# Performance work log

Measured on AMD Instinct MI355X. Metric: run time of the kernel, lower is better.

## Reference

```python
import jax, jax.numpy as jnp
import numpy as np

EMB_SZ = 1024
NUM_HEADS = 16
HEAD_SIZE = EMB_SZ // NUM_HEADS  # 64; inputs must have last dim == HEAD_SIZE (module quirk)
B, S = 2, 2048


def setup_inputs() -> dict:
    key = jax.random.key(0)
    ks = jax.random.split(key, 8)
    return {
        "inputs_for_keys": jax.random.normal(ks[0], (B, S, HEAD_SIZE), jnp.float32),
        "inputs_for_values": jax.random.normal(ks[1], (B, S, HEAD_SIZE), jnp.float32),
        "inputs_for_queries": jax.random.normal(ks[2], (B, S, HEAD_SIZE), jnp.float32),
        # per-head projection weights, stacked over heads (glorot-ish scale)
        "Wk": jax.random.normal(ks[3], (NUM_HEADS, HEAD_SIZE, HEAD_SIZE), jnp.float32) * 0.125,
        "Wv": jax.random.normal(ks[4], (NUM_HEADS, HEAD_SIZE, HEAD_SIZE), jnp.float32) * 0.125,
        "Wq": jax.random.normal(ks[5], (NUM_HEADS, HEAD_SIZE, HEAD_SIZE), jnp.float32) * 0.125,
        "Wo": jax.random.normal(ks[6], (EMB_SZ, EMB_SZ), jnp.float32) * 0.03,
        "bo": jnp.zeros((EMB_SZ,), jnp.float32),
    }


def reference(inputs_for_keys, inputs_for_values, inputs_for_queries, Wk, Wv, Wq, Wo, bo):
    # Each head sees the SAME full inputs (module quirk), distinct weights per head.
    K = jnp.einsum('bsd,hde->bhse', inputs_for_keys, Wk)      # [B,H,Sk,hs]
    V = jnp.einsum('bsd,hde->bhse', inputs_for_values, Wv)    # [B,H,Sk,hs]
    Q = jnp.einsum('bsd,hde->bhse', inputs_for_queries, Wq)   # [B,H,Sq,hs]

    Sq, Sk = Q.shape[2], K.shape[2]
    scores = jnp.einsum('bhqe,bhke->bhqk', Q, K)              # [B,H,Sq,Sk]
    # causal additive mask: -inf strictly above the diagonal (as in np.triu(..., k=1))
    mask = jnp.triu(jnp.full((Sq, Sk), -jnp.inf, dtype=scores.dtype), k=1)
    scale = jnp.asarray(Sk, scores.dtype) ** 0.5
    # NOTE: original divides AFTER adding the mask; -inf/scale == -inf so math matches
    attn = jax.nn.softmax((scores + mask) / scale, axis=-1)   # [B,H,Sq,Sk]

    heads = jnp.einsum('bhqk,bhke->bhqe', attn, V)            # [B,H,Sq,hs]
    # concat heads along last dim (head order matches the Python-loop concat)
    concat = heads.transpose(0, 2, 1, 3).reshape(heads.shape[0], Sq, -1)  # [B,Sq,emb]
    return concat @ Wo + bo                                   # Dense(emb_sz), linear activation
```

## Files before the change

kernel.cpp:

```cpp
#include <hip/hip_runtime.h>
#include <hip/hip_bf16.h>
#include <cstdint>

typedef unsigned short u16;
typedef __bf16 bf16x8 __attribute__((ext_vector_type(8)));
typedef u16 u16x8 __attribute__((ext_vector_type(8)));
typedef unsigned u32x4 __attribute__((ext_vector_type(4)));
typedef float f32x4 __attribute__((ext_vector_type(4)));
typedef float f32x16 __attribute__((ext_vector_type(16)));

#define B_ 2
#define S_ 2048
#define H_ 16
#define HS_ 64
#define EMB_ 1024
#define QSCALE 0.022097086912079608f
#define LOG2E  1.4426950408889634f

static __device__ __forceinline__ u16 f2bf(float f) {
  unsigned int u = __float_as_uint(f);
  u += 0x7fffu + ((u >> 16) & 1u);
  return (u16)(u >> 16);
}

static __device__ __forceinline__ float ex2(float x) {
#if __has_builtin(__builtin_amdgcn_exp2f)
  return __builtin_amdgcn_exp2f(x);
#else
  float r; asm("v_exp_f32 %0, %1" : "=v"(r) : "v"(x)); return r;
#endif
}

static __device__ __forceinline__ float tsum16(const f32x16& s) {
  float a0 = s[0] + s[1],  a1 = s[2] + s[3];
  float a2 = s[4] + s[5],  a3 = s[6] + s[7];
  float a4 = s[8] + s[9],  a5 = s[10] + s[11];
  float a6 = s[12] + s[13], a7 = s[14] + s[15];
  a0 += a1; a2 += a3; a4 += a5; a6 += a7;
  a0 += a2; a4 += a6;
  return a0 + a4;
}

static __device__ __forceinline__ f32x4 mfma16(u16x8 a, u16x8 b, f32x4 c) {
  return __builtin_amdgcn_mfma_f32_16x16x32_bf16(
      __builtin_bit_cast(bf16x8, a), __builtin_bit_cast(bf16x8, b), c, 0, 0, 0);
}
static __device__ __forceinline__ f32x16 mfma32(u16x8 a, u16x8 b, f32x16 c) {
  return __builtin_amdgcn_mfma_f32_32x32x16_bf16(
      __builtin_bit_cast(bf16x8, a), __builtin_bit_cast(bf16x8, b), c, 0, 0, 0);
}

static __device__ __forceinline__ char* swzb(void* base, int row, int colbyte) {
  return (char*)base + ((row * 128 + colbyte) ^ ((row & 7) << 4));
}
static __device__ __forceinline__ u16x8* swzp(void* base, int row, int colbyte) {
  return (u16x8*)swzb(base, row, colbyte);
}

static __device__ __forceinline__ void pk_swap(float a0, float a1, float b0, float b1,
                                               unsigned& x, unsigned& y) {
  unsigned A, Bv;
  asm("v_cvt_pk_bf16_f32 %0, %1, %2" : "=v"(A) : "v"(a0), "v"(a1));
  asm("v_cvt_pk_bf16_f32 %0, %1, %2" : "=v"(Bv) : "v"(b0), "v"(b1));
  asm("v_permlane32_swap_b32 %0, %1" : "+v"(A), "+v"(Bv));
  x = A; y = Bv;
}

__global__ __launch_bounds__(256) void k_transpose_wo(const float* __restrict__ Wo,
                                                      u16* __restrict__ Wot) {
  __shared__ __align__(16) u16 T[64][72];
  const int kb = blockIdx.y * 64, nb = blockIdx.x * 64;
  const int r = threadIdx.x >> 2;
  const int c0 = (threadIdx.x & 3) << 4;
  const float* src = Wo + (size_t)(kb + r) * EMB_ + nb + c0;
#pragma unroll
  for (int i = 0; i < 16; i += 4) {
    float4 f = *(const float4*)(src + i);
    T[c0 + i + 0][r] = f2bf(f.x);
    T[c0 + i + 1][r] = f2bf(f.y);
    T[c0 + i + 2][r] = f2bf(f.z);
    T[c0 + i + 3][r] = f2bf(f.w);
  }
  __syncthreads();
  u16* dst = Wot + (size_t)(nb + r) * EMB_ + kb + c0;
  *(u16x8*)(dst)     = *(const u16x8*)&T[r][c0];
  *(u16x8*)(dst + 8) = *(const u16x8*)&T[r][c0 + 8];
}

__global__ __launch_bounds__(256) void k_proj(
    const float* __restrict__ xq, const float* __restrict__ xk, const float* __restrict__ xv,
    const float* __restrict__ Wq, const float* __restrict__ Wk, const float* __restrict__ Wv,
    u16* __restrict__ Qf, u16* __restrict__ Kf, u16* __restrict__ Vf) {
  __shared__ __align__(16) u16 Xb[64][64];
  __shared__ __align__(16) u16 Wb[64][64];
  __shared__ __align__(16) u16 Tt[64][64];
  const int sb = blockIdx.x;
  const int bh = blockIdx.y;
  const int tn = blockIdx.z;
  const int b = bh >> 4, h = bh & 15;
  const int t = threadIdx.x;
  const int r = t >> 2, c0 = (t & 3) << 4;
  const int lane = t & 63, wv = t >> 6;
  const int lq = lane & 15, lg = lane >> 4;
  const int l31 = lane & 31, hi = lane >> 5;
  const float* xs = (tn == 0) ? xq : (tn == 1) ? xk : xv;
  const float* wsp3 = (tn == 0) ? Wq : (tn == 1) ? Wk : Wv;

  const float* src = xs + ((size_t)(b * S_ + sb * 64 + r)) * HS_ + c0;
#pragma unroll
  for (int i = 0; i < 16; i += 8) {
    float4 fa = *(const float4*)(src + i);
    float4 fb = *(const float4*)(src + i + 4);
    u16x8 v = {f2bf(fa.x), f2bf(fa.y), f2bf(fa.z), f2bf(fa.w),
               f2bf(fb.x), f2bf(fb.y), f2bf(fb.z), f2bf(fb.w)};
    *swzp(Xb, r, (c0 + i) * 2) = v;
  }
  const float* wsp = wsp3 + ((size_t)(h * HS_ + r)) * HS_ + c0;
#pragma unroll
  for (int i = 0; i < 16; i += 4) {
    float4 f = *(const float4*)(wsp + i);
    *(u16*)swzb(Wb, c0 + i + 0, r * 2) = f2bf(f.x);
    *(u16*)swzb(Wb, c0 + i + 1, r * 2) = f2bf(f.y);
    *(u16*)swzb(Wb, c0 + i + 2, r * 2) = f2bf(f.z);
    *(u16*)swzb(Wb, c0 + i + 3, r * 2) = f2bf(f.w);
  }
  __syncthreads();
  if (tn < 2) {
    u16x8 a0 = *swzp(Xb, wv * 16 + lq, lg * 16);
    u16x8 a1 = *swzp(Xb, wv * 16 + lq, 64 + lg * 16);
    const float osc = (tn == 0) ? (QSCALE * LOG2E) : 1.0f;
#pragma unroll
    for (int et = 0; et < 4; ++et) {
      u16x8 b0 = *swzp(Wb, et * 16 + lq, lg * 16);
      u16x8 b1 = *swzp(Wb, et * 16 + lq, 64 + lg * 16);
      f32x4 acc = {0.f, 0.f, 0.f, 0.f};
      acc = mfma16(a0, b0, acc);
      acc = mfma16(a1, b1, acc);
#pragma unroll
      for (int rr = 0; rr < 4; ++rr)
        *(u16*)swzb(Tt, wv * 16 + lg * 4 + rr, (et * 16 + lq) * 2) = f2bf(acc[rr] * osc);
    }
  } else {
    u16x8 xb0 = *swzp(Xb, wv * 16 + lq, lg * 16);
    u16x8 xb1 = *swzp(Xb, wv * 16 + lq, 64 + lg * 16);
#pragma unroll
    for (int et = 0; et < 4; ++et) {
      u16x8 a0 = *swzp(Wb, et * 16 + lq, lg * 16);
      u16x8 a1 = *swzp(Wb, et * 16 + lq, 64 + lg * 16);
      f32x4 acc = {0.f, 0.f, 0.f, 0.f};
      acc = mfma16(a0, xb0, acc);
      acc = mfma16(a1, xb1, acc);
#pragma unroll
      for (int rr = 0; rr < 4; ++rr)
        *(u16*)swzb(Tt, et * 16 + lg * 4 + rr, (wv * 16 + lq) * 2) = f2bf(acc[rr]);
    }
  }
  __syncthreads();
  if (tn < 2) {
    u16* dst = (tn == 0) ? Qf : Kf;
#pragma unroll
    for (int tl = 0; tl < 2; ++tl) {
      u16x8 v = *swzp(Tt, tl * 32 + l31, wv * 32 + hi * 16);
      size_t off = (((size_t)(bh * 64 + sb * 2 + tl)) * 4 + wv) * 512 + lane * 8;
      *(u16x8*)(dst + off) = v;
    }
  } else {
#pragma unroll
    for (int eta = 0; eta < 2; ++eta) {
      u16x8 v = *swzp(Tt, eta * 32 + l31, wv * 32 + hi * 16);
      size_t off = ((((size_t)(bh * 32 + sb)) * 2 + eta) * 4 + wv) * 512 + lane * 8;
      *(u16x8*)(Vf + off) = v;
    }
  }
}

__global__ __launch_bounds__(128, 2) void k_attn(
    const u16* __restrict__ Qf, const u16* __restrict__ Kf, const u16* __restrict__ Vf,
    u16* __restrict__ Co) {
  __shared__ float Xch[64][33];
  __shared__ __align__(16) u16 Osw[32][64];
  const int bid = blockIdx.x;
  const int xcd = bid & 7, idx = bid >> 3;
  const int bh = (xcd << 2) | (idx & 3);
  const int pr = idx >> 2;
  const int b = bh >> 4, h = bh & 15;
  const int w = threadIdx.x >> 6;
  const int l = threadIdx.x & 63;
  const int lq = l & 31, hi = l >> 5;
  const float NEG = -3.0e38f;

  const u16* Kbase = Kf + ((size_t)(bh * 64) * 4) * 512 + l * 8;
  const u16* Vbase = Vf + ((size_t)(bh * 32) * 8) * 512 + l * 8;

#pragma unroll 1
  for (int ph = 0; ph < 2; ++ph) {
    const int t = ph ? (63 - pr) : pr;
    const int qg = t * 32 + lq;
    const int n = (t >> 1) + 1;
    const int mid = n >> 1;
    const int jbeg = w ? mid : 0;
    const int jhot = w ? (n - 1) : mid;

    const u16* Qbase = Qf + (((size_t)(bh * 64 + t)) * 4) * 512 + l * 8;
    u16x8 qf[4];
#pragma unroll
    for (int ss = 0; ss < 4; ++ss) qf[ss] = *(const u16x8*)(Qbase + ss * 512);

    f32x16 o0, o1;
#pragma unroll
    for (int r = 0; r < 16; ++r) { o0[r] = 0.f; o1[r] = 0.f; }
    float ll = 0.f;

    u16x8 kl[4], kh[4], vl[4], vh[4];
    {
      const u16* pk = Kbase + (size_t)jbeg * 8 * 512;
      const u16* pv = Vbase + (size_t)jbeg * 8 * 512;
#pragma unroll
      for (int ss = 0; ss < 4; ++ss) {
        kl[ss] = *(const u16x8*)(pk + ss * 512);
        kh[ss] = *(const u16x8*)(pk + (4 + ss) * 512);
        vl[ss] = *(const u16x8*)(pv + ss * 512);
        vh[ss] = *(const u16x8*)(pv + (4 + ss) * 512);
      }
    }

    for (int j = jbeg; j < jhot; ++j) {
      f32x16 s0, s1;
#pragma unroll
      for (int r = 0; r < 16; ++r) { s0[r] = -16.f; s1[r] = -16.f; }
      __builtin_amdgcn_s_setprio(1);
      s0 = mfma32(kl[0], qf[0], s0);
      s0 = mfma32(kl[1], qf[1], s0);
      s0 = mfma32(kl[2], qf[2], s0);
      s0 = mfma32(kl[3], qf[3], s0);
      s1 = mfma32(kh[0], qf[0], s1);
      s1 = mfma32(kh[1], qf[1], s1);
      s1 = mfma32(kh[2], qf[2], s1);
      s1 = mfma32(kh[3], qf[3], s1);
      __builtin_amdgcn_s_setprio(0);
      {
        const u16* pk = Kbase + (size_t)(j + 1) * 8 * 512;
#pragma unroll
        for (int ss = 0; ss < 4; ++ss) {
          kl[ss] = *(const u16x8*)(pk + ss * 512);
          kh[ss] = *(const u16x8*)(pk + (4 + ss) * 512);
        }
      }
#pragma unroll
      for (int r = 0; r < 16; ++r) s0[r] = ex2(s0[r]);
#pragma unroll
      for (int r = 0; r < 16; ++r) s1[r] = ex2(s1[r]);
      u16x8 pf0, pf1, pf2, pf3;
      {
        unsigned w0, w1, w2, w3;
        pk_swap(s0[0], s0[1], s0[4], s0[5], w0, w2);
        pk_swap(s0[2], s0[3], s0[6], s0[7], w1, w3);
        pf0 = __builtin_bit_cast(u16x8, (u32x4){w0, w1, w2, w3});
        pk_swap(s0[8], s0[9], s0[12], s0[13], w0, w2);
        pk_swap(s0[10], s0[11], s0[14], s0[15], w1, w3);
        pf1 = __builtin_bit_cast(u16x8, (u32x4){w0, w1, w2, w3});
        pk_swap(s1[0], s1[1], s1[4], s1[5], w0, w2);
        pk_swap(s1[2], s1[3], s1[6], s1[7], w1, w3);
        pf2 = __builtin_bit_cast(u16x8, (u32x4){w0, w1, w2, w3});
        pk_swap(s1[8], s1[9], s1[12], s1[13], w0, w2);
        pk_swap(s1[10], s1[11], s1[14], s1[15], w1, w3);
        pf3 = __builtin_bit_cast(u16x8, (u32x4){w0, w1, w2, w3});
      }
      __builtin_amdgcn_s_setprio(1);
      o0 = mfma32(vl[0], pf0, o0);
      o1 = mfma32(vh[0], pf0, o1);
      o0 = mfma32(vl[1], pf1, o0);
      o1 = mfma32(vh[1], pf1, o1);
      o0 = mfma32(vl[2], pf2, o0);
      o1 = mfma32(vh[2], pf2, o1);
      o0 = mfma32(vl[3], pf3, o0);
      o1 = mfma32(vh[3], pf3, o1);
      __builtin_amdgcn_s_setprio(0);
      {
        const u16* pv = Vbase + (size_t)(j + 1) * 8 * 512;
#pragma unroll
        for (int ss = 0; ss < 4; ++ss) {
          vl[ss] = *(const u16x8*)(pv + ss * 512);
          vh[ss] = *(const u16x8*)(pv + (4 + ss) * 512);
        }
      }
      ll += tsum16(s0) + tsum16(s1);
    }

    if (w) {
      const int j = n - 1;
      f32x16 s0, s1;
#pragma unroll
      for (int r = 0; r < 16; ++r) { s0[r] = -16.f; s1[r] = -16.f; }
      s0 = mfma32(kl[0], qf[0], s0);
      s0 = mfma32(kl[1], qf[1], s0);
      s0 = mfma32(kl[2], qf[2], s0);
      s0 = mfma32(kl[3], qf[3], s0);
      if (t & 1) {
        s1 = mfma32(kh[0], qf[0], s1);
        s1 = mfma32(kh[1], qf[1], s1);
        s1 = mfma32(kh[2], qf[2], s1);
        s1 = mfma32(kh[3], qf[3], s1);
      }
      if (t & 1) {
#pragma unroll
        for (int r = 0; r < 16; ++r) {
          int kv = j * 64 + 32 + (r & 3) + 8 * (r >> 2) + 4 * hi;
          if (kv > qg) s1[r] = NEG;
        }
      } else {
#pragma unroll
        for (int r = 0; r < 16; ++r) {
          int kv = j * 64 + (r & 3) + 8 * (r >> 2) + 4 * hi;
          if (kv > qg) s0[r] = NEG;
        }
      }
#pragma unroll
      for (int r = 0; r < 16; ++r) s0[r] = ex2(s0[r]);
      ll += tsum16(s0);
      if (t & 1) {
#pragma unroll
        for (int r = 0; r < 16; ++r) s1[r] = ex2(s1[r]);
        ll += tsum16(s1);
      }
      u16x8 pf0, pf1, pf2, pf3;
      {
        unsigned w0, w1, w2, w3;
        pk_swap(s0[0], s0[1], s0[4], s0[5], w0, w2);
        pk_swap(s0[2], s0[3], s0[6], s0[7], w1, w3);
        pf0 = __builtin_bit_cast(u16x8, (u32x4){w0, w1, w2, w3});
        pk_swap(s0[8], s0[9], s0[12], s0[13], w0, w2);
        pk_swap(s0[10], s0[11], s0[14], s0[15], w1, w3);
        pf1 = __builtin_bit_cast(u16x8, (u32x4){w0, w1, w2, w3});
        if (t & 1) {
          pk_swap(s1[0], s1[1], s1[4], s1[5], w0, w2);
          pk_swap(s1[2], s1[3], s1[6], s1[7], w1, w3);
          pf2 = __builtin_bit_cast(u16x8, (u32x4){w0, w1, w2, w3});
          pk_swap(s1[8], s1[9], s1[12], s1[13], w0, w2);
          pk_swap(s1[10], s1[11], s1[14], s1[15], w1, w3);
          pf3 = __builtin_bit_cast(u16x8, (u32x4){w0, w1, w2, w3});
        }
      }
      o0 = mfma32(vl[0], pf0, o0);
      o1 = mfma32(vh[0], pf0, o1);
      o0 = mfma32(vl[1], pf1, o0);
      o1 = mfma32(vh[1], pf1, o1);
      if (t & 1) {
        o0 = mfma32(vl[2], pf2, o0);
        o1 = mfma32(vh[2], pf2, o1);
        o0 = mfma32(vl[3], pf3, o0);
        o1 = mfma32(vh[3], pf3, o1);
      }
#pragma unroll
      for (int r = 0; r < 16; ++r) { Xch[l][r] = o0[r]; Xch[l][16 + r] = o1[r]; }
      Xch[l][32] = ll;
    }
    __syncthreads();
    if (w == 0) {
#pragma unroll
      for (int r = 0; r < 16; ++r) { o0[r] += Xch[l][r]; o1[r] += Xch[l][16 + r]; }
      ll += Xch[l][32];
      ll += __shfl_xor(ll, 32);
      float inv = 1.0f / ll;
#pragma unroll
      for (int r = 0; r < 16; ++r) {
        int drow = (r & 3) + 8 * (r >> 2) + 4 * hi;
        *(u16*)swzb(Osw, lq, drow * 2) = f2bf(o0[r] * inv);
        *(u16*)swzb(Osw, lq, (32 + drow) * 2) = f2bf(o1[r] * inv);
      }
      u16* dst = Co + ((size_t)(b * S_ + qg)) * EMB_ + h * HS_ + hi * 32;
#pragma unroll
      for (int k = 0; k < 4; ++k) {
        u16x8 vv = *swzp(Osw, lq, (hi * 32 + k * 8) * 2);
        *(u16x8*)(dst + k * 8) = vv;
      }
    }
    __syncthreads();
  }
}

__global__ __launch_bounds__(256) void k_outproj(
    const u16* __restrict__ Cc, const u16* __restrict__ Wot,
    const float* __restrict__ bo, float* __restrict__ out) {
  __shared__ __align__(16) u16 As[64][64];
  __shared__ __align__(16) u16 Bs[128][64];
  const int bid = blockIdx.x;
  const int xcd = bid & 7, sl = bid >> 3;
  const int mb = (xcd << 3) | (sl >> 3);
  const int nb = sl & 7;
  const int t = threadIdx.x;
  const int lane = t & 63, wv = t >> 6;
  const int lq = lane & 15, lg = lane >> 4;
  const int wr = wv >> 1, wc = wv & 1;
  const int srA = t >> 2, scA = (t & 3) << 4;
  const int srB = t >> 1, scB = (t & 1) << 5;
  f32x4 acc[2][4];
#pragma unroll
  for (int mi = 0; mi < 2; ++mi)
#pragma unroll
    for (int ni = 0; ni < 4; ++ni) { f32x4 z = {0.f, 0.f, 0.f, 0.f}; acc[mi][ni] = z; }
  const u16* abase = Cc + ((size_t)(mb * 64 + srA)) * EMB_ + scA;
  const u16* bbase = Wot + ((size_t)(nb * 128 + srB)) * EMB_ + scB;
  u16x8 ar[2], br[4];
#pragma unroll
  for (int q = 0; q < 2; ++q) ar[q] = *(const u16x8*)(abase + q * 8);
#pragma unroll
  for (int q = 0; q < 4; ++q) br[q] = *(const u16x8*)(bbase + q * 8);
  for (int kt = 0; kt < 16; ++kt) {
    __syncthreads();
#pragma unroll
    for (int q = 0; q < 2; ++q) *swzp(As, srA, (scA + q * 8) * 2) = ar[q];
#pragma unroll
    for (int q = 0; q < 4; ++q) *swzp(Bs, srB, (scB + q * 8) * 2) = br[q];
    __syncthreads();
    if (kt < 15) {
#pragma unroll
      for (int q = 0; q < 2; ++q) ar[q] = *(const u16x8*)(abase + (kt + 1) * 64 + q * 8);
#pragma unroll
      for (int q = 0; q < 4; ++q) br[q] = *(const u16x8*)(bbase + (kt + 1) * 64 + q * 8);
    }
#pragma unroll
    for (int kf = 0; kf < 2; ++kf) {
      u16x8 af[2], bf[4];
#pragma unroll
      for (int mi = 0; mi < 2; ++mi)
        af[mi] = *swzp(As, wr * 32 + mi * 16 + lq, kf * 64 + lg * 16);
#pragma unroll
      for (int ni = 0; ni < 4; ++ni)
        bf[ni] = *swzp(Bs, wc * 64 + ni * 16 + lq, kf * 64 + lg * 16);
#pragma unroll
      for (int mi = 0; mi < 2; ++mi)
#pragma unroll
        for (int ni = 0; ni < 4; ++ni)
          acc[mi][ni] = mfma16(af[mi], bf[ni], acc[mi][ni]);
    }
  }
#pragma unroll
  for (int mi = 0; mi < 2; ++mi) {
#pragma unroll
    for (int ni = 0; ni < 4; ++ni) {
      int col = nb * 128 + wc * 64 + ni * 16 + lq;
      float bv = bo[col];
#pragma unroll
      for (int rr = 0; rr < 4; ++rr) {
        int row = mb * 64 + wr * 32 + mi * 16 + lg * 4 + rr;
        out[(size_t)row * EMB_ + col] = acc[mi][ni][rr] + bv;
      }
    }
  }
}

extern "C" void kernel_launch(void* const* d_in, const int* in_sizes, int n_in,
                              void* d_out, int out_size, void* d_ws, size_t ws_size,
                              hipStream_t stream) {
  const float* xk = (const float*)d_in[0];
  const float* xv = (const float*)d_in[1];
  const float* xq = (const float*)d_in[2];
  const float* Wk = (const float*)d_in[3];
  const float* Wv = (const float*)d_in[4];
  const float* Wq = (const float*)d_in[5];
  const float* Wo = (const float*)d_in[6];
  const float* bo = (const float*)d_in[7];
  float* out = (float*)d_out;
  char* ws = (char*)d_ws;
  const size_t MB8 = (size_t)8 * 1024 * 1024;
  u16* Qfw = (u16*)(ws);
  u16* Kfw = (u16*)(ws + MB8);
  u16* Vfw = (u16*)(ws + 2 * MB8);
  u16* Cw  = (u16*)(ws + 3 * MB8);
  u16* Wot = (u16*)(ws + 4 * MB8);

  k_transpose_wo<<<dim3(16, 16), 256, 0, stream>>>(Wo, Wot);
  k_proj<<<dim3(32, 32, 3), 256, 0, stream>>>(xq, xk, xv, Wq, Wk, Wv, Qfw, Kfw, Vfw);
  k_attn<<<1024, 128, 0, stream>>>(Qfw, Kfw, Vfw, Cw);
  k_outproj<<<512, 256, 0, stream>>>(Cw, Wot, bo, out);
}
```

Baseline: 65.34 us.

## Process two query tiles per attention block with four-way KV split

Each attention block now handles a 64-row query tile (two 32-row halves) instead of one 32-row tile, so every K/V fragment loaded is reused for both halves. The KV range is split across four waves instead of two, and partial outputs are reduced through a larger shared-memory exchange. Grid size halves and block size doubles. This cuts K/V global traffic per query row but raises register pressure and shared-memory use, and makes the final reduction heavier.

```diff
diff --git a/kernel.cpp b/kernel.cpp
--- a/kernel.cpp
+++ b/kernel.cpp
@@ -6,6 +6,7 @@
 typedef __bf16 bf16x8 __attribute__((ext_vector_type(8)));
 typedef u16 u16x8 __attribute__((ext_vector_type(8)));
 typedef unsigned u32x4 __attribute__((ext_vector_type(4)));
+typedef float f32x2 __attribute__((ext_vector_type(2)));
 typedef float f32x4 __attribute__((ext_vector_type(4)));
 typedef float f32x16 __attribute__((ext_vector_type(16)));
 
@@ -64,6 +65,21 @@
   asm("v_cvt_pk_bf16_f32 %0, %1, %2" : "=v"(Bv) : "v"(b0), "v"(b1));
   asm("v_permlane32_swap_b32 %0, %1" : "+v"(A), "+v"(Bv));
   x = A; y = Bv;
+}
+
+static __device__ __forceinline__ void pack2(const f32x16& s0, u16x8& pf0, u16x8& pf1) {
+  unsigned w0, w1, w2, w3;
+  pk_swap(s0[0], s0[1], s0[4], s0[5], w0, w2);
+  pk_swap(s0[2], s0[3], s0[6], s0[7], w1, w3);
+  pf0 = __builtin_bit_cast(u16x8, (u32x4){w0, w1, w2, w3});
+  pk_swap(s0[8], s0[9], s0[12], s0[13], w0, w2);
+  pk_swap(s0[10], s0[11], s0[14], s0[15], w1, w3);
+  pf1 = __builtin_bit_cast(u16x8, (u32x4){w0, w1, w2, w3});
+}
+static __device__ __forceinline__ void pack4(const f32x16& s0, const f32x16& s1,
+                                             u16x8& pf0, u16x8& pf1, u16x8& pf2, u16x8& pf3) {
+  pack2(s0, pf0, pf1);
+  pack2(s1, pf2, pf3);
 }
 
 __global__ __launch_bounds__(256) void k_transpose_wo(const float* __restrict__ Wo,
@@ -174,15 +190,16 @@
   }
 }
 
-__global__ __launch_bounds__(128, 2) void k_attn(
+__global__ __launch_bounds__(256, 2) void k_attn(
     const u16* __restrict__ Qf, const u16* __restrict__ Kf, const u16* __restrict__ Vf,
     u16* __restrict__ Co) {
-  __shared__ float Xch[64][33];
-  __shared__ __align__(16) u16 Osw[32][64];
+  __shared__ float Xch[3][64][66];
+  __shared__ __align__(16) u16 OswE[32][64];
+  __shared__ __align__(16) u16 OswO[32][64];
   const int bid = blockIdx.x;
   const int xcd = bid & 7, idx = bid >> 3;
   const int bh = (xcd << 2) | (idx & 3);
-  const int pr = idx >> 2;
+  const int p = idx >> 2;
   const int b = bh >> 4, h = bh & 15;
   const int w = threadIdx.x >> 6;
   const int l = threadIdx.x & 63;
@@ -194,27 +211,29 @@
 
 #pragma unroll 1
   for (int ph = 0; ph < 2; ++ph) {
-    const int t = ph ? (63 - pr) : pr;
-    const int qg = t * 32 + lq;
-    const int n = (t >> 1) + 1;
-    const int mid = n >> 1;
-    const int jbeg = w ? mid : 0;
-    const int jhot = w ? (n - 1) : mid;
-
-    const u16* Qbase = Qf + (((size_t)(bh * 64 + t)) * 4) * 512 + l * 8;
-    u16x8 qf[4];
-#pragma unroll
-    for (int ss = 0; ss < 4; ++ss) qf[ss] = *(const u16x8*)(Qbase + ss * 512);
-
-    f32x16 o0, o1;
-#pragma unroll
-    for (int r = 0; r < 16; ++r) { o0[r] = 0.f; o1[r] = 0.f; }
-    float ll = 0.f;
+    const int g = ph ? (31 - p) : p;
+    const int n = g + 1;
+    const int js = (w * n) >> 2;
+    const int je = ((w + 1) * n) >> 2;
+    const int jhot = (w == 3) ? (n - 1) : je;
+
+    const u16* Qe = Qf + (((size_t)(bh * 64 + 2 * g)) * 4) * 512 + l * 8;
+    u16x8 qfe[4], qfo[4];
+#pragma unroll
+    for (int ss = 0; ss < 4; ++ss) {
+      qfe[ss] = *(const u16x8*)(Qe + ss * 512);
+      qfo[ss] = *(const u16x8*)(Qe + (4 + ss) * 512);
+    }
+
+    f32x16 o0e, o1e, o0o, o1o;
+#pragma unroll
+    for (int r = 0; r < 16; ++r) { o0e[r] = 0.f; o1e[r] = 0.f; o0o[r] = 0.f; o1o[r] = 0.f; }
+    float lle = 0.f, llo = 0.f;
 
     u16x8 kl[4], kh[4], vl[4], vh[4];
-    {
-      const u16* pk = Kbase + (size_t)jbeg * 8 * 512;
-      const u16* pv = Vbase + (size_t)jbeg * 8 * 512;
+    if (js < je) {
+      const u16* pk = Kbase + (size_t)js * 8 * 512;
+      const u16* pv = Vbase + (size_t)js * 8 * 512;
 #pragma unroll
       for (int ss = 0; ss < 4; ++ss) {
         kl[ss] = *(const u16x8*)(pk + ss * 512);
@@ -224,155 +243,205 @@
       }
     }
 
-    for (int j = jbeg; j < jhot; ++j) {
-      f32x16 s0, s1;
-#pragma unroll
-      for (int r = 0; r < 16; ++r) { s0[r] = -16.f; s1[r] = -16.f; }
-      __builtin_amdgcn_s_setprio(1);
-      s0 = mfma32(kl[0], qf[0], s0);
-      s0 = mfma32(kl[1], qf[1], s0);
-      s0 = mfma32(kl[2], qf[2], s0);
-      s0 = mfma32(kl[3], qf[3], s0);
-      s1 = mfma32(kh[0], qf[0], s1);
-      s1 = mfma32(kh[1], qf[1], s1);
-      s1 = mfma32(kh[2], qf[2], s1);
-      s1 = mfma32(kh[3], qf[3], s1);
-      __builtin_amdgcn_s_setprio(0);
-      {
-        const u16* pk = Kbase + (size_t)(j + 1) * 8 * 512;
-#pragma unroll
-        for (int ss = 0; ss < 4; ++ss) {
-          kl[ss] = *(const u16x8*)(pk + ss * 512);
-          kh[ss] = *(const u16x8*)(pk + (4 + ss) * 512);
-        }
-      }
-#pragma unroll
-      for (int r = 0; r < 16; ++r) s0[r] = ex2(s0[r]);
-#pragma unroll
-      for (int r = 0; r < 16; ++r) s1[r] = ex2(s1[r]);
+    for (int j = js; j < jhot; ++j) {
+      const bool pre = (j + 1 < jhot) || (w == 3);
       u16x8 pf0, pf1, pf2, pf3;
       {
-        unsigned w0, w1, w2, w3;
-        pk_swap(s0[0], s0[1], s0[4], s0[5], w0, w2);
-        pk_swap(s0[2], s0[3], s0[6], s0[7], w1, w3);
-        pf0 = __builtin_bit_cast(u16x8, (u32x4){w0, w1, w2, w3});
-        pk_swap(s0[8], s0[9], s0[12], s0[13], w0, w2);
-        pk_swap(s0[10], s0[11], s0[14], s0[15], w1, w3);
-        pf1 = __builtin_bit_cast(u16x8, (u32x4){w0, w1, w2, w3});
-        pk_swap(s1[0], s1[1], s1[4], s1[5], w0, w2);
-        pk_swap(s1[2], s1[3], s1[6], s1[7], w1, w3);
-        pf2 = __builtin_bit_cast(u16x8, (u32x4){w0, w1, w2, w3});
-        pk_swap(s1[8], s1[9], s1[12], s1[13], w0, w2);
-        pk_swap(s1[10], s1[11], s1[14], s1[15], w1, w3);
-        pf3 = __builtin_bit_cast(u16x8, (u32x4){w0, w1, w2, w3});
-      }
-      __builtin_amdgcn_s_setprio(1);
-      o0 = mfma32(vl[0], pf0, o0);
-      o1 = mfma32(vh[0], pf0, o1);
-      o0 = mfma32(vl[1], pf1, o0);
-      o1 = mfma32(vh[1], pf1, o1);
-      o0 = mfma32(vl[2], pf2, o0);
-      o1 = mfma32(vh[2], pf2, o1);
-      o0 = mfma32(vl[3], pf3, o0);
-      o1 = mfma32(vh[3], pf3, o1);
-      __builtin_amdgcn_s_setprio(0);
+        f32x16 s0, s1;
+#pragma unroll
+        for (int r = 0; r < 16; ++r) { s0[r] = -16.f; s1[r] = -16.f; }
+        __builtin_amdgcn_s_setprio(1);
+        s0 = mfma32(kl[0], qfe[0], s0);
+        s0 = mfma32(kl[1], qfe[1], s0);
+        s0 = mfma32(kl[2], qfe[2], s0);
+        s0 = mfma32(kl[3], qfe[3], s0);
+        s1 = mfma32(kh[0], qfe[0], s1);
+        s1 = mfma32(kh[1], qfe[1], s1);
+        s1 = mfma32(kh[2], qfe[2], s1);
+        s1 = mfma32(kh[3], qfe[3], s1);
+        __builtin_amdgcn_s_setprio(0);
+#pragma unroll
+        for (int r = 0; r < 16; ++r) s0[r] = ex2(s0[r]);
+#pragma unroll
+        for (int r = 0; r < 16; ++r) s1[r] = ex2(s1[r]);
+        lle += tsum16(s0) + tsum16(s1);
+        pack4(s0, s1, pf0, pf1, pf2, pf3);
+        __builtin_amdgcn_s_setprio(1);
+        o0e = mfma32(vl[0], pf0, o0e);
+        o1e = mfma32(vh[0], pf0, o1e);
+        o0e = mfma32(vl[1], pf1, o0e);
+        o1e = mfma32(vh[1], pf1, o1e);
+        o0e = mfma32(vl[2], pf2, o0e);
+        o1e = mfma32(vh[2], pf2, o1e);
+        o0e = mfma32(vl[3], pf3, o0e);
+        o1e = mfma32(vh[3], pf3, o1e);
+        __builtin_amdgcn_s_setprio(0);
+      }
       {
-        const u16* pv = Vbase + (size_t)(j + 1) * 8 * 512;
-#pragma unroll
-        for (int ss = 0; ss < 4; ++ss) {
-          vl[ss] = *(const u16x8*)(pv + ss * 512);
-          vh[ss] = *(const u16x8*)(pv + (4 + ss) * 512);
-        }
-      }
-      ll += tsum16(s0) + tsum16(s1);
-    }
-
-    if (w) {
-      const int j = n - 1;
-      f32x16 s0, s1;
-#pragma unroll
-      for (int r = 0; r < 16; ++r) { s0[r] = -16.f; s1[r] = -16.f; }
-      s0 = mfma32(kl[0], qf[0], s0);
-      s0 = mfma32(kl[1], qf[1], s0);
-      s0 = mfma32(kl[2], qf[2], s0);
-      s0 = mfma32(kl[3], qf[3], s0);
-      if (t & 1) {
-        s1 = mfma32(kh[0], qf[0], s1);
-        s1 = mfma32(kh[1], qf[1], s1);
-        s1 = mfma32(kh[2], qf[2], s1);
-        s1 = mfma32(kh[3], qf[3], s1);
-      }
-      if (t & 1) {
-#pragma unroll
-        for (int r = 0; r < 16; ++r) {
-          int kv = j * 64 + 32 + (r & 3) + 8 * (r >> 2) + 4 * hi;
-          if (kv > qg) s1[r] = NEG;
-        }
-      } else {
-#pragma unroll
-        for (int r = 0; r < 16; ++r) {
-          int kv = j * 64 + (r & 3) + 8 * (r >> 2) + 4 * hi;
-          if (kv > qg) s0[r] = NEG;
-        }
-      }
-#pragma unroll
-      for (int r = 0; r < 16; ++r) s0[r] = ex2(s0[r]);
-      ll += tsum16(s0);
-      if (t & 1) {
+        f32x16 s0, s1;
+#pragma unroll
+        for (int r = 0; r < 16; ++r) { s0[r] = -16.f; s1[r] = -16.f; }
+        __builtin_amdgcn_s_setprio(1);
+        s0 = mfma32(kl[0], qfo[0], s0);
+        s0 = mfma32(kl[1], qfo[1], s0);
+        s0 = mfma32(kl[2], qfo[2], s0);
+        s0 = mfma32(kl[3], qfo[3], s0);
+        s1 = mfma32(kh[0], qfo[0], s1);
+        s1 = mfma32(kh[1], qfo[1], s1);
+        s1 = mfma32(kh[2], qfo[2], s1);
+        s1 = mfma32(kh[3], qfo[3], s1);
+        __builtin_amdgcn_s_setprio(0);
+        if (pre) {
+          const u16* pk = Kbase + (size_t)(j + 1) * 8 * 512;
+#pragma unroll
+          for (int ss = 0; ss < 4; ++ss) {
+            kl[ss] = *(const u16x8*)(pk + ss * 512);
+            kh[ss] = *(const u16x8*)(pk + (4 + ss) * 512);
+          }
+        }
+#pragma unroll
+        for (int r = 0; r < 16; ++r) s0[r] = ex2(s0[r]);
 #pragma unroll
         for (int r = 0; r < 16; ++r) s1[r] = ex2(s1[r]);
-        ll += tsum16(s1);
-      }
+        llo += tsum16(s0) + tsum16(s1);
+        pack4(s0, s1, pf0, pf1, pf2, pf3);
+        __builtin_amdgcn_s_setprio(1);
+        o0o = mfma32(vl[0], pf0, o0o);
+        o1o = mfma32(vh[0], pf0, o1o);
+        o0o = mfma32(vl[1], pf1, o0o);
+        o1o = mfma32(vh[1], pf1, o1o);
+        o0o = mfma32(vl[2], pf2, o0o);
+        o1o = mfma32(vh[2], pf2, o1o);
+        o0o = mfma32(vl[3], pf3, o0o);
+        o1o = mfma32(vh[3], pf3, o1o);
+        __builtin_amdgcn_s_setprio(0);
+        if (pre) {
+          const u16* pv = Vbase + (size_t)(j + 1) * 8 * 512;
+#pragma unroll
+          for (int ss = 0; ss < 4; ++ss) {
+            vl[ss] = *(const u16x8*)(pv + ss * 512);
+            vh[ss] = *(const u16x8*)(pv + (4 + ss) * 512);
+          }
+        }
+      }
+    }
+
+    if (w == 3) {
       u16x8 pf0, pf1, pf2, pf3;
       {
-        unsigned w0, w1, w2, w3;
-        pk_swap(s0[0], s0[1], s0[4], s0[5], w0, w2);
-        pk_swap(s0[2], s0[3], s0[6], s0[7], w1, w3);
-        pf0 = __builtin_bit_cast(u16x8, (u32x4){w0, w1, w2, w3});
-        pk_swap(s0[8], s0[9], s0[12], s0[13], w0, w2);
-        pk_swap(s0[10], s0[11], s0[14], s0[15], w1, w3);
-        pf1 = __builtin_bit_cast(u16x8, (u32x4){w0, w1, w2, w3});
-        if (t & 1) {
-          pk_swap(s1[0], s1[1], s1[4], s1[5], w0, w2);
-          pk_swap(s1[2], s1[3], s1[6], s1[7], w1, w3);
-          pf2 = __builtin_bit_cast(u16x8, (u32x4){w0, w1, w2, w3});
-          pk_swap(s1[8], s1[9], s1[12], s1[13], w0, w2);
-          pk_swap(s1[10], s1[11], s1[14], s1[15], w1, w3);
-          pf3 = __builtin_bit_cast(u16x8, (u32x4){w0, w1, w2, w3});
-        }
-      }
-      o0 = mfma32(vl[0], pf0, o0);
-      o1 = mfma32(vh[0], pf0, o1);
-      o0 = mfma32(vl[1], pf1, o0);
-      o1 = mfma32(vh[1], pf1, o1);
-      if (t & 1) {
-        o0 = mfma32(vl[2], pf2, o0);
-        o1 = mfma32(vh[2], pf2, o1);
-        o0 = mfma32(vl[3], pf3, o0);
-        o1 = mfma32(vh[3], pf3, o1);
-      }
-#pragma unroll
-      for (int r = 0; r < 16; ++r) { Xch[l][r] = o0[r]; Xch[l][16 + r] = o1[r]; }
-      Xch[l][32] = ll;
+        f32x16 s0;
+#pragma unroll
+        for (int r = 0; r < 16; ++r) s0[r] = -16.f;
+        s0 = mfma32(kl[0], qfe[0], s0);
+        s0 = mfma32(kl[1], qfe[1], s0);
+        s0 = mfma32(kl[2], qfe[2], s0);
+        s0 = mfma32(kl[3], qfe[3], s0);
+#pragma unroll
+        for (int r = 0; r < 16; ++r) {
+          int crow = (r & 3) + 8 * (r >> 2) + 4 * hi;
+          if (crow > lq) s0[r] = NEG;
+        }
+#pragma unroll
+        for (int r = 0; r < 16; ++r) s0[r] = ex2(s0[r]);
+        lle += tsum16(s0);
+        pack2(s0, pf0, pf1);
+        o0e = mfma32(vl[0], pf0, o0e);
+        o1e = mfma32(vh[0], pf0, o1e);
+        o0e = mfma32(vl[1], pf1, o0e);
+        o1e = mfma32(vh[1], pf1, o1e);
+      }
+      {
+        f32x16 s0, s1;
+#pragma unroll
+        for (int r = 0; r < 16; ++r) { s0[r] = -16.f; s1[r] = -16.f; }
+        s0 = mfma32(kl[0], qfo[0], s0);
+        s0 = mfma32(kl[1], qfo[1], s0);
+        s0 = mfma32(kl[2], qfo[2], s0);
+        s0 = mfma32(kl[3], qfo[3], s0);
+        s1 = mfma32(kh[0], qfo[0], s1);
+        s1 = mfma32(kh[1], qfo[1], s1);
+        s1 = mfma32(kh[2], qfo[2], s1);
+        s1 = mfma32(kh[3], qfo[3], s1);
+#pragma unroll
+        for (int r = 0; r < 16; ++r) {
+          int crow = (r & 3) + 8 * (r >> 2) + 4 * hi;
+          if (crow > lq) s1[r] = NEG;
+        }
+#pragma unroll
+        for (int r = 0; r < 16; ++r) s0[r] = ex2(s0[r]);
+#pragma unroll
+        for (int r = 0; r < 16; ++r) s1[r] = ex2(s1[r]);
+        llo += tsum16(s0) + tsum16(s1);
+        pack4(s0, s1, pf0, pf1, pf2, pf3);
+        o0o = mfma32(vl[0], pf0, o0o);
+        o1o = mfma32(vh[0], pf0, o1o);
+        o0o = mfma32(vl[1], pf1, o0o);
+        o1o = mfma32(vh[1], pf1, o1o);
+        o0o = mfma32(vl[2], pf2, o0o);
+        o1o = mfma32(vh[2], pf2, o1o);
+        o0o = mfma32(vl[3], pf3, o0o);
+        o1o = mfma32(vh[3], pf3, o1o);
+      }
+    }
+
+    if (w) {
+      f32x2* xr = (f32x2*)(&Xch[w - 1][l][0]);
+#pragma unroll
+      for (int i = 0; i < 8; ++i) {
+        xr[i]      = (f32x2){o0e[2 * i], o0e[2 * i + 1]};
+        xr[8 + i]  = (f32x2){o1e[2 * i], o1e[2 * i + 1]};
+        xr[16 + i] = (f32x2){o0o[2 * i], o0o[2 * i + 1]};
+        xr[24 + i] = (f32x2){o1o[2 * i], o1o[2 * i + 1]};
+      }
+      xr[32] = (f32x2){lle, llo};
     }
     __syncthreads();
     if (w == 0) {
 #pragma unroll
-      for (int r = 0; r < 16; ++r) { o0[r] += Xch[l][r]; o1[r] += Xch[l][16 + r]; }
-      ll += Xch[l][32];
-      ll += __shfl_xor(ll, 32);
-      float inv = 1.0f / ll;
-#pragma unroll
-      for (int r = 0; r < 16; ++r) {
-        int drow = (r & 3) + 8 * (r >> 2) + 4 * hi;
-        *(u16*)swzb(Osw, lq, drow * 2) = f2bf(o0[r] * inv);
-        *(u16*)swzb(Osw, lq, (32 + drow) * 2) = f2bf(o1[r] * inv);
-      }
-      u16* dst = Co + ((size_t)(b * S_ + qg)) * EMB_ + h * HS_ + hi * 32;
-#pragma unroll
-      for (int k = 0; k < 4; ++k) {
-        u16x8 vv = *swzp(Osw, lq, (hi * 32 + k * 8) * 2);
-        *(u16x8*)(dst + k * 8) = vv;
+      for (int wv = 0; wv < 3; ++wv) {
+        const f32x2* xr = (const f32x2*)(&Xch[wv][l][0]);
+#pragma unroll
+        for (int i = 0; i < 8; ++i) {
+          f32x2 a = xr[i], bq = xr[8 + i], c = xr[16 + i], d = xr[24 + i];
+          o0e[2 * i] += a[0]; o0e[2 * i + 1] += a[1];
+          o1e[2 * i] += bq[0]; o1e[2 * i + 1] += bq[1];
+          o0o[2 * i] += c[0]; o0o[2 * i + 1] += c[1];
+          o1o[2 * i] += d[0]; o1o[2 * i + 1] += d[1];
+        }
+        f32x2 e = xr[32];
+        lle += e[0]; llo += e[1];
+      }
+      lle += __shfl_xor(lle, 32);
+      llo += __shfl_xor(llo, 32);
+      {
+        float inv = 1.0f / lle;
+#pragma unroll
+        for (int r = 0; r < 16; ++r) {
+          int drow = (r & 3) + 8 * (r >> 2) + 4 * hi;
+          *(u16*)swzb(OswE, lq, drow * 2) = f2bf(o0e[r] * inv);
+          *(u16*)swzb(OswE, lq, (32 + drow) * 2) = f2bf(o1e[r] * inv);
+        }
+        u16* dst = Co + ((size_t)(b * S_ + 64 * g + lq)) * EMB_ + h * HS_ + hi * 32;
+#pragma unroll
+        for (int k = 0; k < 4; ++k) {
+          u16x8 vv = *swzp(OswE, lq, (hi * 32 + k * 8) * 2);
+          *(u16x8*)(dst + k * 8) = vv;
+        }
+      }
+      {
+        float inv = 1.0f / llo;
+#pragma unroll
+        for (int r = 0; r < 16; ++r) {
+          int drow = (r & 3) + 8 * (r >> 2) + 4 * hi;
+          *(u16*)swzb(OswO, lq, drow * 2) = f2bf(o0o[r] * inv);
+          *(u16*)swzb(OswO, lq, (32 + drow) * 2) = f2bf(o1o[r] * inv);
+        }
+        u16* dst = Co + ((size_t)(b * S_ + 64 * g + 32 + lq)) * EMB_ + h * HS_ + hi * 32;
+#pragma unroll
+        for (int k = 0; k < 4; ++k) {
+          u16x8 vv = *swzp(OswO, lq, (hi * 32 + k * 8) * 2);
+          *(u16x8*)(dst + k * 8) = vv;
+        }
       }
     }
     __syncthreads();
@@ -472,6 +541,6 @@
 
   k_transpose_wo<<<dim3(16, 16), 256, 0, stream>>>(Wo, Wot);
   k_proj<<<dim3(32, 32, 3), 256, 0, stream>>>(xq, xk, xv, Wq, Wk, Wv, Qfw, Kfw, Vfw);
-  k_attn<<<1024, 128, 0, stream>>>(Qfw, Kfw, Vfw, Cw);
+  k_attn<<<512, 256, 0, stream>>>(Qfw, Kfw, Vfw, Cw);
   k_outproj<<<512, 256, 0, stream>>>(Cw, Wot, bo, out);
 }
```

After: 69.69 us. 1.07x slower.
